# Performance work log

Measured on AMD Instinct MI355X. Metric: run time of the kernel, lower is better.

The kernel has to match this reference:

```python
import jax, jax.numpy as jnp
import numpy as np

H_SIZE = 768
N_HEADS = 12
HEAD_DIM = H_SIZE // N_HEADS  # 64
WINDOW = 64
BATCH = 2
SEQ = 1024


def setup_inputs() -> dict:
    key = jax.random.key(0)
    ks = jax.random.split(key, 9)
    s = 1.0 / np.sqrt(H_SIZE)
    return {
        "hidden_states": jax.random.normal(ks[0], (BATCH, SEQ, H_SIZE), jnp.float32),
        "Wq": jax.random.normal(ks[1], (H_SIZE, H_SIZE), jnp.float32) * s,
        "bq": jnp.zeros((H_SIZE,), jnp.float32),
        "Wk": jax.random.normal(ks[2], (H_SIZE, H_SIZE), jnp.float32) * s,
        "bk": jnp.zeros((H_SIZE,), jnp.float32),
        "Wv": jax.random.normal(ks[3], (H_SIZE, H_SIZE), jnp.float32) * s,
        "bv": jnp.zeros((H_SIZE,), jnp.float32),
        "Wo": jax.random.normal(ks[4], (H_SIZE, H_SIZE), jnp.float32) * s,
        "bo": jnp.zeros((H_SIZE,), jnp.float32),
    }


def _heads(x):
    # [B,S,H*d] -> [B,H,S,d]
    B, S, _ = x.shape
    return x.reshape(B, S, N_HEADS, HEAD_DIM).transpose(0, 2, 1, 3)


def reference(hidden_states, Wq, bq, Wk, bk, Wv, bv, Wo, bo):
    B, S, _ = hidden_states.shape
    q = _heads(hidden_states @ Wq.T + bq)  # [B,H,S,d]
    k = _heads(hidden_states @ Wk.T + bk)
    v = _heads(hidden_states @ Wv.T + bv)

    half = WINDOW // 2
    # zero-pad keys/values along sequence so every query has a full window
    # (mirrors the module's F.pad with value=0; padded keys score 0 in softmax)
    kp = jnp.pad(k, ((0, 0), (0, 0), (half, half), (0, 0)))  # [B,H,S+W,d]
    vp = jnp.pad(v, ((0, 0), (0, 0), (half, half), (0, 0)))

    # window gather indices: query i attends padded positions i..i+W-1
    idx = jnp.arange(S)[:, None] + jnp.arange(WINDOW)[None, :]  # [S,W]
    kw = kp[:, :, idx, :]  # [B,H,S,W,d]
    vw = vp[:, :, idx, :]

    scale = 1.0 / jnp.sqrt(jnp.asarray(HEAD_DIM, hidden_states.dtype))
    scores = jnp.einsum("bhsd,bhswd->bhsw", q, kw) * scale
    probs = jax.nn.softmax(scores, axis=-1)  # dropout inactive (eval mode)
    ctx = jnp.einsum("bhsw,bhswd->bhsd", probs, vw)  # [B,H,S,d]

    ctx = ctx.transpose(0, 2, 1, 3).reshape(B, S, N_HEADS * HEAD_DIM)
    return ctx @ Wo.T + bo
```

## Files before the change

### kernel.cpp

```cpp
#include <hip/hip_runtime.h>
#include <hip/hip_bf16.h>

typedef __bf16 bf16x8 __attribute__((ext_vector_type(8)));
typedef float f32x4 __attribute__((ext_vector_type(4)));
typedef unsigned short u16;

#define H_SZ 768
#define NH 12
#define SEQ 1024

__device__ __forceinline__ u16 f2b(float f) {
  unsigned u = __builtin_bit_cast(unsigned, f);
  unsigned r = (u + 0x7FFFu + ((u >> 16) & 1u)) >> 16;
  return (u16)r;
}

#define GLL16(g, l)                                                            \
  __builtin_amdgcn_global_load_lds(                                            \
      (const __attribute__((address_space(1))) void*)(g),                      \
      (__attribute__((address_space(3))) void*)(l), 16, 0, 0)

#define WQKV_OFF 0u
#define KW_OFF 3538944u
#define VW_OFF 6684672u
#define WO_OFF 9830400u
#define CTX_OFF 0u
#define XB_OUT_OFF 0u
#define QW_OUT_OFF 3145728u


__global__ __launch_bounds__(256) void prep_kernel(
    const float* __restrict__ hs, const float* __restrict__ wq,
    const float* __restrict__ wk, const float* __restrict__ wv,
    const float* __restrict__ wo, u16* __restrict__ xb,
    u16* __restrict__ wqkvb, u16* __restrict__ wob) {
  int c = blockIdx.x * 256 + threadIdx.x;
  const float* src;
  u16* dst;
  if (c < 393216) {
    src = hs + (size_t)c * 4; dst = xb + (size_t)c * 4;
  } else if (c < 540672) {
    int i = c - 393216; src = wq + (size_t)i * 4; dst = wqkvb + (size_t)i * 4;
  } else if (c < 688128) {
    int i = c - 540672; src = wk + (size_t)i * 4; dst = wqkvb + 589824 + (size_t)i * 4;
  } else if (c < 835584) {
    int i = c - 688128; src = wv + (size_t)i * 4; dst = wqkvb + 1179648 + (size_t)i * 4;
  } else {
    int i = c - 835584; src = wo + (size_t)i * 4; dst = wob + (size_t)i * 4;
  }
  float4 v = *(const float4*)src;
  ushort4 o;
  o.x = f2b(v.x); o.y = f2b(v.y); o.z = f2b(v.z); o.w = f2b(v.w);
  *(ushort4*)dst = o;
}

template <int MODE, int TM, int TN, int BK>
__global__ __launch_bounds__(256) void gemm_bt(
    const u16* __restrict__ A, const u16* __restrict__ Bm, int K,
    const float* __restrict__ b0, const float* __restrict__ b1,
    const float* __restrict__ b2, u16* __restrict__ oq, u16* __restrict__ ok,
    u16* __restrict__ ov, float* __restrict__ of) {
  constexpr int MI = TM / 32;
  constexpr int NJ = TN / 32;
  constexpr int KS = BK / 32;
  constexpr int CPR = BK / 8;
  constexpr int CMASK = CPR - 1;
  constexpr int CHA = TM * CPR / 256;
  constexpr int CHB = TN * CPR / 256;
  __shared__ u16 As[2][TM * BK];
  __shared__ u16 Bs[2][TN * BK];
  const int tid = threadIdx.x;
  const int lane = tid & 63;
  const int wave = tid >> 6;
  const int wm = (wave & 1) * (TM / 2), wn = (wave >> 1) * (TN / 2);
  const int lrow = lane & 15, quad = lane >> 4;

  const u16* Ab = A + (size_t)blockIdx.y * TM * K;
  const u16* Bb = Bm + (size_t)blockIdx.x * TN * K;

  int ar[CHA], ac[CHA];
#pragma unroll
  for (int c = 0; c < CHA; c++) {
    int bi = tid + c * 256;
    ar[c] = bi / CPR;
    ac[c] = ((bi & CMASK) ^ (ar[c] & CMASK)) * 8;
  }
  int br[CHB], bc[CHB];
#pragma unroll
  for (int c = 0; c < CHB; c++) {
    int bi = tid + c * 256;
    br[c] = bi / CPR;
    bc[c] = ((bi & CMASK) ^ (br[c] & CMASK)) * 8;
  }

  f32x4 acc[MI][NJ] = {};

#pragma unroll
  for (int c = 0; c < CHA; c++)
    GLL16(Ab + (size_t)ar[c] * K + ac[c], &As[0][(tid + c * 256) * 8]);
#pragma unroll
  for (int c = 0; c < CHB; c++)
    GLL16(Bb + (size_t)br[c] * K + bc[c], &Bs[0][(tid + c * 256) * 8]);

  int cur = 0;
  for (int kt = 0; kt < K; kt += BK) {
    __syncthreads();
    const int nxt = cur ^ 1;
    if (kt + BK < K) {
#pragma unroll
      for (int c = 0; c < CHA; c++)
        GLL16(Ab + (size_t)ar[c] * K + kt + BK + ac[c],
              &As[nxt][(tid + c * 256) * 8]);
#pragma unroll
      for (int c = 0; c < CHB; c++)
        GLL16(Bb + (size_t)br[c] * K + kt + BK + bc[c],
              &Bs[nxt][(tid + c * 256) * 8]);
    }
#pragma unroll
    for (int ks = 0; ks < KS; ks++) {
      bf16x8 af[MI], bf[NJ];
#pragma unroll
      for (int i = 0; i < MI; i++) {
        int row = wm + i * 16 + lrow;
        int lc = (ks * 4 + quad) ^ (row & CMASK);
        af[i] = *(const bf16x8*)&As[cur][row * BK + lc * 8];
      }
#pragma unroll
      for (int j = 0; j < NJ; j++) {
        int row = wn + j * 16 + lrow;
        int lc = (ks * 4 + quad) ^ (row & CMASK);
        bf[j] = *(const bf16x8*)&Bs[cur][row * BK + lc * 8];
      }
#pragma unroll
      for (int i = 0; i < MI; i++)
#pragma unroll
        for (int j = 0; j < NJ; j++)
          acc[i][j] = __builtin_amdgcn_mfma_f32_16x16x32_bf16(
              af[i], bf[j], acc[i][j], 0, 0, 0);
    }
    cur = nxt;
  }

  if (MODE == 0) {
#pragma unroll
    for (int j = 0; j < NJ; j++) {
      int nbase = blockIdx.x * TN + wn + j * 16;
      int sec = (nbase >= 1536) ? 2 : (nbase >= 768 ? 1 : 0);
      int nn = nbase - sec * 768 + lrow;
      const float* bp = (sec == 0) ? b0 : (sec == 1 ? b1 : b2);
      u16* dst = (sec == 0) ? oq : (sec == 1 ? ok : ov);
      float bias = bp[nn];
      int h = nn >> 6, d = nn & 63;
#pragma unroll
      for (int i = 0; i < MI; i++) {
        int mbase = blockIdx.y * TM + wm + i * 16 + quad * 4;
#pragma unroll
        for (int r = 0; r < 4; r++) {
          int mm = mbase + r;
          int plane = (mm >> 10) * NH + h;
          dst[((size_t)(plane << 10) + (mm & 1023)) * 64 + d] =
              f2b(acc[i][j][r] + bias);
        }
      }
    }
  } else {
#pragma unroll
    for (int j = 0; j < NJ; j++) {
      int n = blockIdx.x * TN + wn + j * 16 + lrow;
      float bias = b0[n];
#pragma unroll
      for (int i = 0; i < MI; i++) {
        int mbase = blockIdx.y * TM + wm + i * 16 + quad * 4;
#pragma unroll
        for (int r = 0; r < 4; r++) {
          int mm = mbase + r;
          of[(size_t)mm * H_SZ + n] = acc[i][j][r] + bias;
        }
      }
    }
  }
}

__global__ __launch_bounds__(256) void attn_kernel(
    const u16* __restrict__ qw, const u16* __restrict__ kw,
    const u16* __restrict__ vw, u16* __restrict__ ctx) {
  __shared__ u16 VT[64][136];
  __shared__ u16 P[4][16][136];
  const int tid = threadIdx.x;
  const int lane = tid & 63;
  const int wave = tid >> 6;
  const int lrow = lane & 15, quad = lane >> 4;
  const int bh = blockIdx.x;
  const int qb = blockIdx.y;
  const int s0 = qb * 64;
  const int b = bh / NH, h = bh - b * NH;

  const u16* qp = qw + (size_t)bh * SEQ * 64;
  const u16* kp = kw + (size_t)bh * SEQ * 64;
  const u16* vp = vw + (size_t)bh * SEQ * 64;

  const u16* qbase = qp + (size_t)(s0 + wave * 16 + lrow) * 64 + quad * 8;
  bf16x8 aq0 = *(const bf16x8*)qbase;
  bf16x8 aq1 = *(const bf16x8*)(qbase + 32);
  bf16x8 bk0[8], bk1[8];
#pragma unroll
  for (int nt = 0; nt < 8; nt++) {
    int key = s0 - 32 + nt * 16 + lrow;
    int kc = min(max(key, 0), SEQ - 1);
    const u16* kb = kp + (size_t)kc * 64 + quad * 8;
    bk0[nt] = *(const bf16x8*)kb;
    bk1[nt] = *(const bf16x8*)(kb + 32);
  }

#pragma unroll
  for (int it = 0; it < 4; it++) {
    int chunk = it * 256 + tid;
    int r = chunk & 127;
    int c8 = chunk >> 7;
    int key = s0 - 32 + r;
    uint4 val = make_uint4(0, 0, 0, 0);
    if (key >= 0 && key < SEQ)
      val = *(const uint4*)(vp + (size_t)key * 64 + c8 * 8);
    union { uint4 u; u16 s[8]; } uu;
    uu.u = val;
#pragma unroll
    for (int t = 0; t < 8; t++) VT[c8 * 8 + t][r] = uu.s[t];
  }
  __syncthreads();

  f32x4 sc[8];
#pragma unroll
  for (int nt = 0; nt < 8; nt++) {
    f32x4 c = {0.f, 0.f, 0.f, 0.f};
    c = __builtin_amdgcn_mfma_f32_16x16x32_bf16(aq0, bk0[nt], c, 0, 0, 0);
    c = __builtin_amdgcn_mfma_f32_16x16x32_bf16(aq1, bk1[nt], c, 0, 0, 0);
    sc[nt] = c;
  }

#pragma unroll
  for (int nt = 0; nt < 8; nt++) {
#pragma unroll
    for (int r = 0; r < 4; r++) {
      int j = s0 - 32 + nt * 16 + lrow;
      int i = s0 + wave * 16 + quad * 4 + r;
      int w = j - i + 32;
      float s = sc[nt][r] * 0.125f;
      if (w < 0 || w > 63) s = -1e30f;
      else if (j < 0 || j >= SEQ) s = 0.0f;
      sc[nt][r] = s;
    }
  }

  float linv[4];
#pragma unroll
  for (int r = 0; r < 4; r++) {
    float m = sc[0][r];
#pragma unroll
    for (int nt = 1; nt < 8; nt++) m = fmaxf(m, sc[nt][r]);
    m = fmaxf(m, __shfl_xor(m, 1, 64));
    m = fmaxf(m, __shfl_xor(m, 2, 64));
    m = fmaxf(m, __shfl_xor(m, 4, 64));
    m = fmaxf(m, __shfl_xor(m, 8, 64));
    float l = 0.f;
#pragma unroll
    for (int nt = 0; nt < 8; nt++) {
      float p = __expf(sc[nt][r] - m);
      sc[nt][r] = p;
      l += p;
    }
    l += __shfl_xor(l, 1, 64);
    l += __shfl_xor(l, 2, 64);
    l += __shfl_xor(l, 4, 64);
    l += __shfl_xor(l, 8, 64);
    linv[r] = 1.0f / l;
  }

#pragma unroll
  for (int nt = 0; nt < 8; nt++)
#pragma unroll
    for (int r = 0; r < 4; r++)
      P[wave][quad * 4 + r][nt * 16 + lrow] = f2b(sc[nt][r]);

#pragma unroll
  for (int dt = 0; dt < 4; dt++) {
    f32x4 o = {0.f, 0.f, 0.f, 0.f};
#pragma unroll
    for (int kk = 0; kk < 4; kk++) {
      bf16x8 pa = *(const bf16x8*)&P[wave][lrow][kk * 32 + quad * 8];
      bf16x8 vb = *(const bf16x8*)&VT[dt * 16 + lrow][kk * 32 + quad * 8];
      o = __builtin_amdgcn_mfma_f32_16x16x32_bf16(pa, vb, o, 0, 0, 0);
    }
#pragma unroll
    for (int r = 0; r < 4; r++) {
      int token = b * SEQ + s0 + wave * 16 + quad * 4 + r;
      ctx[(size_t)token * H_SZ + h * 64 + dt * 16 + lrow] =
          f2b(o[r] * linv[r]);
    }
  }
}

extern "C" void kernel_launch(void* const* d_in, const int* in_sizes, int n_in,
                              void* d_out, int out_size, void* d_ws,
                              size_t ws_size, hipStream_t stream) {
  (void)in_sizes; (void)n_in; (void)out_size; (void)ws_size;
  const float* hs = (const float*)d_in[0];
  const float* Wq = (const float*)d_in[1];
  const float* bq = (const float*)d_in[2];
  const float* Wk = (const float*)d_in[3];
  const float* bk = (const float*)d_in[4];
  const float* Wv = (const float*)d_in[5];
  const float* bv = (const float*)d_in[6];
  const float* Wo = (const float*)d_in[7];
  const float* bo = (const float*)d_in[8];
  float* out = (float*)d_out;
  char* ws = (char*)d_ws;
  char* ob = (char*)d_out;
  u16* xb = (u16*)(ob + XB_OUT_OFF);
  u16* qw = (u16*)(ob + QW_OUT_OFF);
  u16* wqkvb = (u16*)(ws + WQKV_OFF);
  u16* kw = (u16*)(ws + KW_OFF);
  u16* vw = (u16*)(ws + VW_OFF);
  u16* wob = (u16*)(ws + WO_OFF);
  u16* ctx = (u16*)(ws + CTX_OFF);

  prep_kernel<<<3840, 256, 0, stream>>>(hs, Wq, Wk, Wv, Wo, xb, wqkvb, wob);
  gemm_bt<0, 64, 128, 64><<<dim3(18, 32), 256, 0, stream>>>(
      xb, wqkvb, 768, bq, bk, bv, qw, kw, vw, nullptr);
  attn_kernel<<<dim3(24, 16), 256, 0, stream>>>(qw, kw, vw, ctx);
  gemm_bt<1, 64, 128, 64><<<dim3(6, 32), 256, 0, stream>>>(
      ctx, wob, 768, bo, nullptr, nullptr, nullptr, nullptr, nullptr, out);
}
```

Measured before the change: 118.3 us.

## Triple-buffer GEMM shared-memory tiles with partial vmcnt waits

Converts the GEMM k-loop from double to triple buffering, prefetching two tiles ahead through global_load_lds. Each iteration waits only for the older tile's loads with a partial vmcnt instead of a full sync, which lets a load stay in flight across the barrier. The cost is 50% more LDS per block, which may reduce occupancy. Correctness relies on the vmcnt count matching the number of loads issued per tile.

```diff
diff --git a/kernel.cpp b/kernel.cpp
--- a/kernel.cpp
+++ b/kernel.cpp
@@ -67,8 +67,8 @@
   constexpr int CMASK = CPR - 1;
   constexpr int CHA = TM * CPR / 256;
   constexpr int CHB = TN * CPR / 256;
-  __shared__ u16 As[2][TM * BK];
-  __shared__ u16 Bs[2][TN * BK];
+  __shared__ u16 As[3][TM * BK];
+  __shared__ u16 Bs[3][TN * BK];
   const int tid = threadIdx.x;
   const int lane = tid & 63;
   const int wave = tid >> 6;
@@ -101,20 +101,34 @@
 #pragma unroll
   for (int c = 0; c < CHB; c++)
     GLL16(Bb + (size_t)br[c] * K + bc[c], &Bs[0][(tid + c * 256) * 8]);
+  if (BK < K) {
+#pragma unroll
+    for (int c = 0; c < CHA; c++)
+      GLL16(Ab + (size_t)ar[c] * K + BK + ac[c], &As[1][(tid + c * 256) * 8]);
+#pragma unroll
+    for (int c = 0; c < CHB; c++)
+      GLL16(Bb + (size_t)br[c] * K + BK + bc[c], &Bs[1][(tid + c * 256) * 8]);
+  }
 
   int cur = 0;
   for (int kt = 0; kt < K; kt += BK) {
-    __syncthreads();
-    const int nxt = cur ^ 1;
-    if (kt + BK < K) {
+    if (kt + BK >= K)
+      asm volatile("s_waitcnt vmcnt(0)" ::: "memory");
+    else
+      asm volatile("s_waitcnt vmcnt(%0)" ::"i"(CHA + CHB) : "memory");
+    __builtin_amdgcn_s_barrier();
+    __builtin_amdgcn_sched_barrier(0);
+    if (kt + 2 * BK < K) {
+      int nb = cur + 2;
+      if (nb >= 3) nb -= 3;
 #pragma unroll
       for (int c = 0; c < CHA; c++)
-        GLL16(Ab + (size_t)ar[c] * K + kt + BK + ac[c],
-              &As[nxt][(tid + c * 256) * 8]);
+        GLL16(Ab + (size_t)ar[c] * K + kt + 2 * BK + ac[c],
+              &As[nb][(tid + c * 256) * 8]);
 #pragma unroll
       for (int c = 0; c < CHB; c++)
-        GLL16(Bb + (size_t)br[c] * K + kt + BK + bc[c],
-              &Bs[nxt][(tid + c * 256) * 8]);
+        GLL16(Bb + (size_t)br[c] * K + kt + 2 * BK + bc[c],
+              &Bs[nb][(tid + c * 256) * 8]);
     }
 #pragma unroll
     for (int ks = 0; ks < KS; ks++) {
@@ -138,7 +152,7 @@
           acc[i][j] = __builtin_amdgcn_mfma_f32_16x16x32_bf16(
               af[i], bf[j], acc[i][j], 0, 0, 0);
     }
-    cur = nxt;
+    cur = (cur == 2) ? 0 : cur + 1;
   }
 
   if (MODE == 0) {
```

New measurement: 126.2 us. 6.7% more time.
